# Optimization experiments

Hardware: AMD Instinct MI355X
Metric: run time of the kernel (lower is better)

The kernel has to match this reference:

```python
import jax, jax.numpy as jnp
import numpy as np

ALPHA = 0.1  # LeakyReLU negative slope
NHEADS, NHID, NFEAT, NCLASS, N = 4, 16, 512, 40, 8192


def _gat_layer(x, adj, W, a):
    """One multi-head GraphAttentionLayer block (all heads vectorized).
    x: [N, Fin], adj: [N, N], W: [H, Fin, Fout], a: [H, 2*Fout].
    NOTE: the source computes an attention softmax but then OVERWRITES it with
    h_prime = adj @ h (dead code). We reproduce the actual output math.
    The (dead) attention, in its efficient decomposed form, would be:
        s1 = einsum('hnf,hf->hn', h, a[:, :Fout])
        s2 = einsum('hnf,hf->hn', h, a[:, Fout:])
        e  = leaky_relu(s1[:, :, None] + s2[:, None, :], ALPHA)
        att = softmax(where(adj[None] > 0, e, -9e15), axis=2)
        h_prime = einsum('hij,hjf->hif', att, h)   # <- discarded by source
    """
    h = jnp.einsum('nf,hfo->hno', x, W)        # [H, N, Fout]
    hp = jnp.einsum('ij,hjf->hif', adj, h)     # source: h_prime = adj @ h
    out = jax.nn.elu(hp)                        # concat=True path
    H, n, Fo = out.shape
    return jnp.transpose(out, (1, 0, 2)).reshape(n, H * Fo)  # cat heads on feat dim


def setup_inputs() -> dict:
    key = jax.random.key(0)
    ks = jax.random.split(key, 8)
    x = jax.random.normal(ks[0], (N, NFEAT), dtype=jnp.float32)
    # sparse-ish binary dense adjacency (adj > 0 mask pattern)
    adj = (jax.random.uniform(ks[1], (N, N)) < 0.01).astype(jnp.float32)
    sc = lambda fan: (2.0 / fan) ** 0.5
    W0 = jax.random.normal(ks[2], (NHEADS, NFEAT, NHID), dtype=jnp.float32) * sc(NFEAT)
    a0 = jax.random.normal(ks[3], (NHEADS, 2 * NHID), dtype=jnp.float32) * sc(2 * NHID)
    W1 = jax.random.normal(ks[4], (NHEADS, NHID * NHEADS, NHID), dtype=jnp.float32) * sc(NHID * NHEADS)
    a1 = jax.random.normal(ks[5], (NHEADS, 2 * NHID), dtype=jnp.float32) * sc(2 * NHID)
    lin_w = jax.random.normal(ks[6], (NHID * NHEADS, NCLASS), dtype=jnp.float32) * sc(NHID * NHEADS)
    lin_b = jnp.zeros((NCLASS,), dtype=jnp.float32)
    return {"x": x, "adj": adj, "W0": W0, "a0": a0, "W1": W1, "a1": a1,
            "lin_w": lin_w, "lin_b": lin_b}


def reference(x, adj, W0, a0, W1, a1, lin_w, lin_b):
    # eval mode: F.dropout is identity
    emb0 = _gat_layer(x, adj, W0, a0)      # [N, NHEADS*NHID]
    emb1 = _gat_layer(emb0, adj, W1, a1)   # [N, NHEADS*NHID]
    out = jax.nn.elu(emb1) @ lin_w + lin_b # [N, NCLASS]
    return (jax.nn.log_softmax(out, axis=1), emb0, emb1, out)
```

## Files before the change

### kernel.cpp

```cpp
#include <hip/hip_runtime.h>
#include <hip/hip_bf16.h>
#include <math.h>

#define NN 8192
#define NFEAT 512
#define NHID 16
#define NHEADS 4
#define FEAT 64
#define NCLASS 40
#define CAP 192

__global__ __launch_bounds__(256) void build_ell(const float* __restrict__ adj,
                                                 unsigned short* __restrict__ ell,
                                                 unsigned int* __restrict__ counts) {
    __shared__ unsigned short buf[CAP];
    __shared__ int cnt;
    int row = blockIdx.x;
    if (threadIdx.x == 0) cnt = 0;
    __syncthreads();
    const float4* a4 = (const float4*)(adj + (size_t)row * NN);
    #pragma unroll
    for (int i = 0; i < NN / 4 / 256; ++i) {
        int idx4 = i * 256 + threadIdx.x;
        float4 v = a4[idx4];
        int cb = idx4 * 4;
        if (v.x != 0.f) { int p = atomicAdd(&cnt, 1); if (p < CAP) buf[p] = (unsigned short)(cb);     }
        if (v.y != 0.f) { int p = atomicAdd(&cnt, 1); if (p < CAP) buf[p] = (unsigned short)(cb + 1); }
        if (v.z != 0.f) { int p = atomicAdd(&cnt, 1); if (p < CAP) buf[p] = (unsigned short)(cb + 2); }
        if (v.w != 0.f) { int p = atomicAdd(&cnt, 1); if (p < CAP) buf[p] = (unsigned short)(cb + 3); }
    }
    __syncthreads();
    int c = cnt < CAP ? cnt : CAP;
    if (threadIdx.x == 0) counts[row] = (unsigned int)c;
    unsigned short* er = ell + (size_t)row * CAP;
    for (int k = threadIdx.x; k < c; k += 256) er[k] = buf[k];
}

__global__ __launch_bounds__(256) void gemm_xw0(const float* __restrict__ x,
                                                const float* __restrict__ W0,
                                                float* __restrict__ h0) {
    __shared__ float xs[16][128];
    __shared__ float ws[128][64];
    int row0 = blockIdx.x * 16;
    int c  = threadIdx.x & 63;
    int rg = threadIdx.x >> 6;
    float acc[4] = {0.f, 0.f, 0.f, 0.f};
    for (int kb = 0; kb < 4; ++kb) {
        const float4* x4 = (const float4*)x;
        #pragma unroll
        for (int i = 0; i < 2; ++i) {
            int f = i * 256 + threadIdx.x;
            int r = f >> 5, k4 = f & 31;
            float4 v = x4[((size_t)(row0 + r) * NFEAT + kb * 128) / 4 + k4];
            xs[r][k4 * 4 + 0] = v.x; xs[r][k4 * 4 + 1] = v.y;
            xs[r][k4 * 4 + 2] = v.z; xs[r][k4 * 4 + 3] = v.w;
        }
        const float4* w4 = (const float4*)W0;
        #pragma unroll
        for (int i = 0; i < 8; ++i) {
            int f = i * 256 + threadIdx.x;
            int kk = f >> 4, c4 = f & 15;
            int h = c4 >> 2, o4 = c4 & 3;
            float4 v = w4[(h * NFEAT * NHID + (kb * 128 + kk) * NHID) / 4 + o4];
            ws[kk][c4 * 4 + 0] = v.x; ws[kk][c4 * 4 + 1] = v.y;
            ws[kk][c4 * 4 + 2] = v.z; ws[kk][c4 * 4 + 3] = v.w;
        }
        __syncthreads();
        for (int kk = 0; kk < 128; ++kk) {
            float wv = ws[kk][c];
            #pragma unroll
            for (int i = 0; i < 4; ++i) acc[i] += xs[rg * 4 + i][kk] * wv;
        }
        __syncthreads();
    }
    #pragma unroll
    for (int i = 0; i < 4; ++i)
        h0[(size_t)(row0 + rg * 4 + i) * FEAT + c] = acc[i];
}

__global__ __launch_bounds__(256) void spmm_elu(const float* __restrict__ h,
                                                const unsigned short* __restrict__ ell,
                                                const unsigned int* __restrict__ counts,
                                                float* __restrict__ emb) {
    int w = threadIdx.x >> 6, lane = threadIdx.x & 63;
    int row = blockIdx.x * 4 + w;
    int cnt = (int)counts[row];
    const unsigned short* ep = ell + (size_t)row * CAP;
    float acc = 0.f;
    int k = 0;
    for (; k + 4 <= cnt; k += 4) {
        int j0 = ep[k], j1 = ep[k + 1], j2 = ep[k + 2], j3 = ep[k + 3];
        float v0 = h[(size_t)j0 * FEAT + lane];
        float v1 = h[(size_t)j1 * FEAT + lane];
        float v2 = h[(size_t)j2 * FEAT + lane];
        float v3 = h[(size_t)j3 * FEAT + lane];
        acc += (v0 + v1) + (v2 + v3);
    }
    for (; k < cnt; ++k) acc += h[(size_t)ep[k] * FEAT + lane];
    emb[(size_t)row * FEAT + lane] = acc > 0.f ? acc : expm1f(acc);
}

__global__ __launch_bounds__(256) void gemm_emb_w1(const float* __restrict__ emb0,
                                                   const float* __restrict__ W1,
                                                   float* __restrict__ h1) {
    __shared__ float es[32][64];
    __shared__ float ws[64][64];
    int row0 = blockIdx.x * 32;
    int c = threadIdx.x & 63;
    int w = threadIdx.x >> 6;
    const float4* e4 = (const float4*)(emb0 + (size_t)row0 * FEAT);
    #pragma unroll
    for (int i = 0; i < 2; ++i) {
        int f = i * 256 + threadIdx.x;
        float4 v = e4[f];
        int r = f >> 4, c4 = f & 15;
        es[r][c4 * 4 + 0] = v.x; es[r][c4 * 4 + 1] = v.y;
        es[r][c4 * 4 + 2] = v.z; es[r][c4 * 4 + 3] = v.w;
    }
    const float4* w4 = (const float4*)W1;
    #pragma unroll
    for (int i = 0; i < 4; ++i) {
        int f = i * 256 + threadIdx.x;
        int j = f >> 4, c4 = f & 15;
        int h = c4 >> 2, o4 = c4 & 3;
        float4 v = w4[(h * FEAT * NHID + j * NHID) / 4 + o4];
        ws[j][c4 * 4 + 0] = v.x; ws[j][c4 * 4 + 1] = v.y;
        ws[j][c4 * 4 + 2] = v.z; ws[j][c4 * 4 + 3] = v.w;
    }
    __syncthreads();
    float acc[8] = {0.f,0.f,0.f,0.f,0.f,0.f,0.f,0.f};
    for (int k = 0; k < 64; ++k) {
        float wv = ws[k][c];
        #pragma unroll
        for (int i = 0; i < 8; ++i) acc[i] += es[w * 8 + i][k] * wv;
    }
    #pragma unroll
    for (int i = 0; i < 8; ++i)
        h1[(size_t)(row0 + w * 8 + i) * FEAT + c] = acc[i];
}

__global__ __launch_bounds__(256) void final_kernel(const float* __restrict__ emb1,
                                                    const float* __restrict__ lin_w,
                                                    const float* __restrict__ lin_b,
                                                    float* __restrict__ out_lsm,
                                                    float* __restrict__ out_raw) {
    __shared__ float sh[4][64];
    int w = threadIdx.x >> 6, lane = threadIdx.x & 63;
    int row = blockIdx.x * 4 + w;
    float v = emb1[(size_t)row * FEAT + lane];
    sh[w][lane] = v > 0.f ? v : expm1f(v);
    __syncthreads();
    float acc = 0.f;
    if (lane < NCLASS) {
        acc = lin_b[lane];
        for (int j = 0; j < FEAT; ++j) acc += sh[w][j] * lin_w[j * NCLASS + lane];
        out_raw[(size_t)row * NCLASS + lane] = acc;
    }
    float m = (lane < NCLASS) ? acc : -INFINITY;
    #pragma unroll
    for (int off = 32; off; off >>= 1) m = fmaxf(m, __shfl_xor(m, off, 64));
    float ex = (lane < NCLASS) ? expf(acc - m) : 0.f;
    float s = ex;
    #pragma unroll
    for (int off = 32; off; off >>= 1) s += __shfl_xor(s, off, 64);
    if (lane < NCLASS)
        out_lsm[(size_t)row * NCLASS + lane] = acc - m - logf(s);
}

extern "C" void kernel_launch(void* const* d_in, const int* in_sizes, int n_in,
                              void* d_out, int out_size, void* d_ws, size_t ws_size,
                              hipStream_t stream) {
    const float* x     = (const float*)d_in[0];
    const float* adj   = (const float*)d_in[1];
    const float* W0    = (const float*)d_in[2];
    const float* W1    = (const float*)d_in[4];
    const float* lin_w = (const float*)d_in[6];
    const float* lin_b = (const float*)d_in[7];

    float* out      = (float*)d_out;
    float* out_lsm  = out;
    float* out_emb0 = out + (size_t)NN * NCLASS;
    float* out_emb1 = out_emb0 + (size_t)NN * FEAT;
    float* out_raw  = out_emb1 + (size_t)NN * FEAT;

    char* ws = (char*)d_ws;
    unsigned int*   counts = (unsigned int*)ws;
    unsigned short* ell    = (unsigned short*)(ws + 32768);
    float* h0 = (float*)(ws + 32768 + (size_t)NN * CAP * 2);
    float* h1 = h0 + (size_t)NN * FEAT;

    build_ell<<<NN, 256, 0, stream>>>(adj, ell, counts);
    gemm_xw0<<<NN / 16, 256, 0, stream>>>(x, W0, h0);
    spmm_elu<<<NN / 4, 256, 0, stream>>>(h0, ell, counts, out_emb0);
    gemm_emb_w1<<<NN / 32, 256, 0, stream>>>(out_emb0, W1, h1);
    spmm_elu<<<NN / 4, 256, 0, stream>>>(h1, ell, counts, out_emb1);
    final_kernel<<<NN / 4, 256, 0, stream>>>(out_emb1, lin_w, lin_b, out_lsm, out_raw);
}
```

Measured before the change: 435.8 us.

## Fuse six kernels into three: merged ELL+GEMM, SpMM+W1, SpMM+final

Merges the ELL build and the x@W0 GEMM into one launch with block-range dispatch. It also fuses the first SpMM+ELU with the emb0@W1 projection per row, and the second SpMM with the ELU, linear layer and log-softmax. The aim is to cut launch overhead and the global round trips of emb0 and emb1, and to overlap the GEMM with the adjacency scan. In exchange, every k2/k3 block reloads W1 or lin_w into shared memory. The SpMM unroll goes from 4 to 8, and the GEMM K-tile shrinks to 64.

```diff
diff --git a/kernel.cpp b/kernel.cpp
--- a/kernel.cpp
+++ b/kernel.cpp
@@ -9,162 +9,167 @@
 #define FEAT 64
 #define NCLASS 40
 #define CAP 192
-
-__global__ __launch_bounds__(256) void build_ell(const float* __restrict__ adj,
-                                                 unsigned short* __restrict__ ell,
-                                                 unsigned int* __restrict__ counts) {
-    __shared__ unsigned short buf[CAP];
-    __shared__ int cnt;
-    int row = blockIdx.x;
-    if (threadIdx.x == 0) cnt = 0;
-    __syncthreads();
-    const float4* a4 = (const float4*)(adj + (size_t)row * NN);
-    #pragma unroll
-    for (int i = 0; i < NN / 4 / 256; ++i) {
-        int idx4 = i * 256 + threadIdx.x;
-        float4 v = a4[idx4];
-        int cb = idx4 * 4;
-        if (v.x != 0.f) { int p = atomicAdd(&cnt, 1); if (p < CAP) buf[p] = (unsigned short)(cb);     }
-        if (v.y != 0.f) { int p = atomicAdd(&cnt, 1); if (p < CAP) buf[p] = (unsigned short)(cb + 1); }
-        if (v.z != 0.f) { int p = atomicAdd(&cnt, 1); if (p < CAP) buf[p] = (unsigned short)(cb + 2); }
-        if (v.w != 0.f) { int p = atomicAdd(&cnt, 1); if (p < CAP) buf[p] = (unsigned short)(cb + 3); }
-    }
-    __syncthreads();
-    int c = cnt < CAP ? cnt : CAP;
-    if (threadIdx.x == 0) counts[row] = (unsigned int)c;
-    unsigned short* er = ell + (size_t)row * CAP;
-    for (int k = threadIdx.x; k < c; k += 256) er[k] = buf[k];
-}
-
-__global__ __launch_bounds__(256) void gemm_xw0(const float* __restrict__ x,
-                                                const float* __restrict__ W0,
-                                                float* __restrict__ h0) {
-    __shared__ float xs[16][128];
-    __shared__ float ws[128][64];
-    int row0 = blockIdx.x * 16;
-    int c  = threadIdx.x & 63;
-    int rg = threadIdx.x >> 6;
-    float acc[4] = {0.f, 0.f, 0.f, 0.f};
-    for (int kb = 0; kb < 4; ++kb) {
+#define GEMM_NB 512
+
+__global__ __launch_bounds__(256) void k1_build_and_gemm(
+        const float* __restrict__ x, const float* __restrict__ W0,
+        const float* __restrict__ adj,
+        unsigned short* __restrict__ ell, unsigned int* __restrict__ counts,
+        float* __restrict__ h0) {
+    if (blockIdx.x < GEMM_NB) {
+        __shared__ float xs[16][64];
+        __shared__ float ws[64][64];
+        int row0 = blockIdx.x * 16;
+        int c  = threadIdx.x & 63;
+        int rg = threadIdx.x >> 6;
+        float acc[4] = {0.f, 0.f, 0.f, 0.f};
         const float4* x4 = (const float4*)x;
+        const float4* w4 = (const float4*)W0;
+        for (int kb = 0; kb < 8; ++kb) {
+            {
+                int r = threadIdx.x >> 4, k4 = threadIdx.x & 15;
+                float4 v = x4[(size_t)(row0 + r) * (NFEAT / 4) + kb * 16 + k4];
+                xs[r][k4 * 4 + 0] = v.x; xs[r][k4 * 4 + 1] = v.y;
+                xs[r][k4 * 4 + 2] = v.z; xs[r][k4 * 4 + 3] = v.w;
+            }
+            #pragma unroll
+            for (int i = 0; i < 4; ++i) {
+                int f = i * 256 + threadIdx.x;
+                int kk = f >> 4, c4 = f & 15;
+                int h = c4 >> 2, o4 = c4 & 3;
+                float4 v = w4[h * (NFEAT * NHID / 4) + (kb * 64 + kk) * (NHID / 4) + o4];
+                ws[kk][c4 * 4 + 0] = v.x; ws[kk][c4 * 4 + 1] = v.y;
+                ws[kk][c4 * 4 + 2] = v.z; ws[kk][c4 * 4 + 3] = v.w;
+            }
+            __syncthreads();
+            for (int kk = 0; kk < 64; ++kk) {
+                float wv = ws[kk][c];
+                #pragma unroll
+                for (int i = 0; i < 4; ++i) acc[i] += xs[rg * 4 + i][kk] * wv;
+            }
+            __syncthreads();
+        }
         #pragma unroll
-        for (int i = 0; i < 2; ++i) {
-            int f = i * 256 + threadIdx.x;
-            int r = f >> 5, k4 = f & 31;
-            float4 v = x4[((size_t)(row0 + r) * NFEAT + kb * 128) / 4 + k4];
-            xs[r][k4 * 4 + 0] = v.x; xs[r][k4 * 4 + 1] = v.y;
-            xs[r][k4 * 4 + 2] = v.z; xs[r][k4 * 4 + 3] = v.w;
-        }
-        const float4* w4 = (const float4*)W0;
+        for (int i = 0; i < 4; ++i)
+            h0[(size_t)(row0 + rg * 4 + i) * FEAT + c] = acc[i];
+    } else {
+        __shared__ unsigned short buf[CAP];
+        __shared__ int cnt;
+        int row = blockIdx.x - GEMM_NB;
+        if (threadIdx.x == 0) cnt = 0;
+        __syncthreads();
+        const float4* a4 = (const float4*)(adj + (size_t)row * NN);
         #pragma unroll
-        for (int i = 0; i < 8; ++i) {
-            int f = i * 256 + threadIdx.x;
-            int kk = f >> 4, c4 = f & 15;
-            int h = c4 >> 2, o4 = c4 & 3;
-            float4 v = w4[(h * NFEAT * NHID + (kb * 128 + kk) * NHID) / 4 + o4];
-            ws[kk][c4 * 4 + 0] = v.x; ws[kk][c4 * 4 + 1] = v.y;
-            ws[kk][c4 * 4 + 2] = v.z; ws[kk][c4 * 4 + 3] = v.w;
+        for (int i = 0; i < NN / 4 / 256; ++i) {
+            int idx4 = i * 256 + threadIdx.x;
+            float4 v = a4[idx4];
+            int cb = idx4 * 4;
+            if (v.x != 0.f) { int p = atomicAdd(&cnt, 1); if (p < CAP) buf[p] = (unsigned short)(cb);     }
+            if (v.y != 0.f) { int p = atomicAdd(&cnt, 1); if (p < CAP) buf[p] = (unsigned short)(cb + 1); }
+            if (v.z != 0.f) { int p = atomicAdd(&cnt, 1); if (p < CAP) buf[p] = (unsigned short)(cb + 2); }
+            if (v.w != 0.f) { int p = atomicAdd(&cnt, 1); if (p < CAP) buf[p] = (unsigned short)(cb + 3); }
         }
         __syncthreads();
-        for (int kk = 0; kk < 128; ++kk) {
-            float wv = ws[kk][c];
-            #pragma unroll
-            for (int i = 0; i < 4; ++i) acc[i] += xs[rg * 4 + i][kk] * wv;
-        }
-        __syncthreads();
-    }
-    #pragma unroll
-    for (int i = 0; i < 4; ++i)
-        h0[(size_t)(row0 + rg * 4 + i) * FEAT + c] = acc[i];
-}
-
-__global__ __launch_bounds__(256) void spmm_elu(const float* __restrict__ h,
-                                                const unsigned short* __restrict__ ell,
-                                                const unsigned int* __restrict__ counts,
-                                                float* __restrict__ emb) {
+        int c = cnt < CAP ? cnt : CAP;
+        if (threadIdx.x == 0) counts[row] = (unsigned int)c;
+        unsigned short* er = ell + (size_t)row * CAP;
+        for (int k = threadIdx.x; k < c; k += 256) er[k] = buf[k];
+    }
+}
+
+__global__ __launch_bounds__(256) void k2_spmm_w1(
+        const float* __restrict__ h0,
+        const unsigned short* __restrict__ ell, const unsigned int* __restrict__ counts,
+        const float* __restrict__ W1,
+        float* __restrict__ emb0_out, float* __restrict__ h1) {
+    __shared__ float w1s[64][64];
+    __shared__ float e0s[4][64];
+    const float4* w4 = (const float4*)W1;
+    #pragma unroll
+    for (int i = 0; i < 4; ++i) {
+        int f = i * 256 + threadIdx.x;
+        int j = f >> 4, c4 = f & 15;
+        float4 v = w4[(c4 >> 2) * (FEAT * NHID / 4) + j * (NHID / 4) + (c4 & 3)];
+        w1s[j][c4 * 4 + 0] = v.x; w1s[j][c4 * 4 + 1] = v.y;
+        w1s[j][c4 * 4 + 2] = v.z; w1s[j][c4 * 4 + 3] = v.w;
+    }
+    __syncthreads();
     int w = threadIdx.x >> 6, lane = threadIdx.x & 63;
     int row = blockIdx.x * 4 + w;
     int cnt = (int)counts[row];
     const unsigned short* ep = ell + (size_t)row * CAP;
     float acc = 0.f;
     int k = 0;
-    for (; k + 4 <= cnt; k += 4) {
-        int j0 = ep[k], j1 = ep[k + 1], j2 = ep[k + 2], j3 = ep[k + 3];
-        float v0 = h[(size_t)j0 * FEAT + lane];
-        float v1 = h[(size_t)j1 * FEAT + lane];
-        float v2 = h[(size_t)j2 * FEAT + lane];
-        float v3 = h[(size_t)j3 * FEAT + lane];
-        acc += (v0 + v1) + (v2 + v3);
-    }
-    for (; k < cnt; ++k) acc += h[(size_t)ep[k] * FEAT + lane];
-    emb[(size_t)row * FEAT + lane] = acc > 0.f ? acc : expm1f(acc);
-}
-
-__global__ __launch_bounds__(256) void gemm_emb_w1(const float* __restrict__ emb0,
-                                                   const float* __restrict__ W1,
-                                                   float* __restrict__ h1) {
-    __shared__ float es[32][64];
-    __shared__ float ws[64][64];
-    int row0 = blockIdx.x * 32;
-    int c = threadIdx.x & 63;
-    int w = threadIdx.x >> 6;
-    const float4* e4 = (const float4*)(emb0 + (size_t)row0 * FEAT);
-    #pragma unroll
-    for (int i = 0; i < 2; ++i) {
-        int f = i * 256 + threadIdx.x;
-        float4 v = e4[f];
-        int r = f >> 4, c4 = f & 15;
-        es[r][c4 * 4 + 0] = v.x; es[r][c4 * 4 + 1] = v.y;
-        es[r][c4 * 4 + 2] = v.z; es[r][c4 * 4 + 3] = v.w;
-    }
-    const float4* w4 = (const float4*)W1;
-    #pragma unroll
-    for (int i = 0; i < 4; ++i) {
-        int f = i * 256 + threadIdx.x;
-        int j = f >> 4, c4 = f & 15;
-        int h = c4 >> 2, o4 = c4 & 3;
-        float4 v = w4[(h * FEAT * NHID + j * NHID) / 4 + o4];
-        ws[j][c4 * 4 + 0] = v.x; ws[j][c4 * 4 + 1] = v.y;
-        ws[j][c4 * 4 + 2] = v.z; ws[j][c4 * 4 + 3] = v.w;
+    for (; k + 8 <= cnt; k += 8) {
+        int j0 = ep[k], j1 = ep[k+1], j2 = ep[k+2], j3 = ep[k+3];
+        int j4 = ep[k+4], j5 = ep[k+5], j6 = ep[k+6], j7 = ep[k+7];
+        float v0 = h0[(size_t)j0 * FEAT + lane], v1 = h0[(size_t)j1 * FEAT + lane];
+        float v2 = h0[(size_t)j2 * FEAT + lane], v3 = h0[(size_t)j3 * FEAT + lane];
+        float v4 = h0[(size_t)j4 * FEAT + lane], v5 = h0[(size_t)j5 * FEAT + lane];
+        float v6 = h0[(size_t)j6 * FEAT + lane], v7 = h0[(size_t)j7 * FEAT + lane];
+        acc += ((v0 + v1) + (v2 + v3)) + ((v4 + v5) + (v6 + v7));
+    }
+    for (; k < cnt; ++k) acc += h0[(size_t)ep[k] * FEAT + lane];
+    float e = acc > 0.f ? acc : expm1f(acc);
+    emb0_out[(size_t)row * FEAT + lane] = e;
+    e0s[w][lane] = e;
+    float h1acc = 0.f;
+    #pragma unroll
+    for (int j = 0; j < 64; ++j) h1acc += e0s[w][j] * w1s[j][lane];
+    h1[(size_t)row * FEAT + lane] = h1acc;
+}
+
+__global__ __launch_bounds__(256) void k3_spmm_final(
+        const float* __restrict__ h1,
+        const unsigned short* __restrict__ ell, const unsigned int* __restrict__ counts,
+        const float* __restrict__ lin_w, const float* __restrict__ lin_b,
+        float* __restrict__ emb1_out, float* __restrict__ out_lsm,
+        float* __restrict__ out_raw) {
+    __shared__ float lws[64][NCLASS];
+    __shared__ float e2s[4][64];
+    const float4* l4 = (const float4*)lin_w;
+    for (int f = threadIdx.x; f < 640; f += 256) {
+        float4 v = l4[f];
+        int j = f / 10, c0 = (f % 10) * 4;
+        lws[j][c0] = v.x; lws[j][c0 + 1] = v.y; lws[j][c0 + 2] = v.z; lws[j][c0 + 3] = v.w;
     }
     __syncthreads();
-    float acc[8] = {0.f,0.f,0.f,0.f,0.f,0.f,0.f,0.f};
-    for (int k = 0; k < 64; ++k) {
-        float wv = ws[k][c];
-        #pragma unroll
-        for (int i = 0; i < 8; ++i) acc[i] += es[w * 8 + i][k] * wv;
-    }
-    #pragma unroll
-    for (int i = 0; i < 8; ++i)
-        h1[(size_t)(row0 + w * 8 + i) * FEAT + c] = acc[i];
-}
-
-__global__ __launch_bounds__(256) void final_kernel(const float* __restrict__ emb1,
-                                                    const float* __restrict__ lin_w,
-                                                    const float* __restrict__ lin_b,
-                                                    float* __restrict__ out_lsm,
-                                                    float* __restrict__ out_raw) {
-    __shared__ float sh[4][64];
     int w = threadIdx.x >> 6, lane = threadIdx.x & 63;
     int row = blockIdx.x * 4 + w;
-    float v = emb1[(size_t)row * FEAT + lane];
-    sh[w][lane] = v > 0.f ? v : expm1f(v);
-    __syncthreads();
+    int cnt = (int)counts[row];
+    const unsigned short* ep = ell + (size_t)row * CAP;
     float acc = 0.f;
+    int k = 0;
+    for (; k + 8 <= cnt; k += 8) {
+        int j0 = ep[k], j1 = ep[k+1], j2 = ep[k+2], j3 = ep[k+3];
+        int j4 = ep[k+4], j5 = ep[k+5], j6 = ep[k+6], j7 = ep[k+7];
+        float v0 = h1[(size_t)j0 * FEAT + lane], v1 = h1[(size_t)j1 * FEAT + lane];
+        float v2 = h1[(size_t)j2 * FEAT + lane], v3 = h1[(size_t)j3 * FEAT + lane];
+        float v4 = h1[(size_t)j4 * FEAT + lane], v5 = h1[(size_t)j5 * FEAT + lane];
+        float v6 = h1[(size_t)j6 * FEAT + lane], v7 = h1[(size_t)j7 * FEAT + lane];
+        acc += ((v0 + v1) + (v2 + v3)) + ((v4 + v5) + (v6 + v7));
+    }
+    for (; k < cnt; ++k) acc += h1[(size_t)ep[k] * FEAT + lane];
+    float e1 = acc > 0.f ? acc : expm1f(acc);
+    emb1_out[(size_t)row * FEAT + lane] = e1;
+    float e2 = e1 > 0.f ? e1 : expm1f(e1);
+    e2s[w][lane] = e2;
+    float o = 0.f;
     if (lane < NCLASS) {
-        acc = lin_b[lane];
-        for (int j = 0; j < FEAT; ++j) acc += sh[w][j] * lin_w[j * NCLASS + lane];
-        out_raw[(size_t)row * NCLASS + lane] = acc;
-    }
-    float m = (lane < NCLASS) ? acc : -INFINITY;
+        o = lin_b[lane];
+        #pragma unroll
+        for (int j = 0; j < 64; ++j) o += e2s[w][j] * lws[j][lane];
+        out_raw[(size_t)row * NCLASS + lane] = o;
+    }
+    float m = (lane < NCLASS) ? o : -INFINITY;
     #pragma unroll
     for (int off = 32; off; off >>= 1) m = fmaxf(m, __shfl_xor(m, off, 64));
-    float ex = (lane < NCLASS) ? expf(acc - m) : 0.f;
+    float ex = (lane < NCLASS) ? expf(o - m) : 0.f;
     float s = ex;
     #pragma unroll
     for (int off = 32; off; off >>= 1) s += __shfl_xor(s, off, 64);
     if (lane < NCLASS)
-        out_lsm[(size_t)row * NCLASS + lane] = acc - m - logf(s);
+        out_lsm[(size_t)row * NCLASS + lane] = o - m - logf(s);
 }
 
 extern "C" void kernel_launch(void* const* d_in, const int* in_sizes, int n_in,
@@ -189,10 +194,8 @@
     float* h0 = (float*)(ws + 32768 + (size_t)NN * CAP * 2);
     float* h1 = h0 + (size_t)NN * FEAT;
 
-    build_ell<<<NN, 256, 0, stream>>>(adj, ell, counts);
-    gemm_xw0<<<NN / 16, 256, 0, stream>>>(x, W0, h0);
-    spmm_elu<<<NN / 4, 256, 0, stream>>>(h0, ell, counts, out_emb0);
-    gemm_emb_w1<<<NN / 32, 256, 0, stream>>>(out_emb0, W1, h1);
-    spmm_elu<<<NN / 4, 256, 0, stream>>>(h1, ell, counts, out_emb1);
-    final_kernel<<<NN / 4, 256, 0, stream>>>(out_emb1, lin_w, lin_b, out_lsm, out_raw);
-}
+    k1_build_and_gemm<<<GEMM_NB + NN, 256, 0, stream>>>(x, W0, adj, ell, counts, h0);
+    k2_spmm_w1<<<NN / 4, 256, 0, stream>>>(h0, ell, counts, W1, out_emb0, h1);
+    k3_spmm_final<<<NN / 4, 256, 0, stream>>>(h1, ell, counts, lin_w, lin_b,
+                                              out_emb1, out_lsm, out_raw);
+}
```

Result: faster. 411.2 us (-5.6%).
